# Performance work log

Measured on AMD Instinct MI355X. Metric: run time of the kernel, lower is better.

## Reference

```python
import jax, jax.numpy as jnp
import numpy as np

IN_DIM = 9
HIDDEN = 32
SORT_K = 30


def setup_inputs() -> dict:
    key = jax.random.key(0)
    ks = jax.random.split(key, 16)
    N, E, G = 250000, 2500000, 2048
    x = jax.random.normal(ks[0], (N, IN_DIM), dtype=jnp.float32)
    edge_index = jax.random.randint(ks[1], (2, E), 0, N, dtype=jnp.int32)
    batch = jnp.sort(jax.random.randint(ks[2], (N,), 0, G, dtype=jnp.int32))
    s = lambda k, sh: jax.random.normal(k, sh, dtype=jnp.float32) * 0.05
    return {
        "x": x, "edge_index": edge_index, "batch": batch, "num_graphs": G,
        "W1": s(ks[3], (IN_DIM, HIDDEN)), "b1": jnp.zeros((HIDDEN,), jnp.float32),
        "W2": s(ks[4], (HIDDEN, HIDDEN)), "b2": jnp.zeros((HIDDEN,), jnp.float32),
        "W3": s(ks[5], (HIDDEN, HIDDEN)), "b3": jnp.zeros((HIDDEN,), jnp.float32),
        "cw1": s(ks[6], (16, HIDDEN, 5)), "cb1": jnp.zeros((16,), jnp.float32),
        "cw2": s(ks[7], (32, 16, 5)), "cb2": jnp.zeros((32,), jnp.float32),
        "lw1": s(ks[8], (32 * (SORT_K - 8), 128)), "lb1": jnp.zeros((128,), jnp.float32),
        "lw2": s(ks[9], (128, 1)), "lb2": jnp.zeros((1,), jnp.float32),
    }


def _gcn(x, W, b, src, dst, dis, n):
    # PyG-style GCNConv: sym-normalized A+I, linear transform first.
    h = x @ W                                     # [N, H]
    msg = h[src] * (dis[src] * dis[dst])[:, None]  # [E, H]
    agg = jax.ops.segment_sum(msg, dst, num_segments=n)
    agg = agg + h * (dis * dis)[:, None]           # self-loops
    return agg + b


def _sort_pool(x, batch, num_graphs, k):
    n, h = x.shape
    key = x[:, -1]
    order = jnp.lexsort((-key, batch))             # by graph, key descending
    xs = x[order]
    bs = batch[order]
    counts = jax.ops.segment_sum(jnp.ones((n,), jnp.int32), batch, num_segments=num_graphs)
    starts = jnp.cumsum(counts) - counts           # exclusive prefix sum
    pos = jnp.arange(n, dtype=jnp.int32) - starts[bs]
    valid = pos < k
    g = jnp.where(valid, bs, num_graphs)           # out-of-range -> dropped
    p = jnp.where(valid, pos, 0)
    out = jnp.zeros((num_graphs, k, h), x.dtype)
    return out.at[g, p].set(xs, mode="drop")


def _conv1d(x, w, b):
    # x: [B, C, T], w: [O, I, K]
    y = jax.lax.conv_general_dilated(x, w, window_strides=(1,), padding="VALID",
                                     dimension_numbers=("NCH", "OIH", "NCH"))
    return y + b[None, :, None]


def reference(x, edge_index, batch, num_graphs, W1, b1, W2, b2, W3, b3,
              cw1, cb1, cw2, cb2, lw1, lb1, lw2, lb2):
    n = x.shape[0]
    src, dst = edge_index[0], edge_index[1]
    deg = jax.ops.segment_sum(jnp.ones_like(src, dtype=x.dtype), dst, num_segments=n) + 1.0
    dis = jax.lax.rsqrt(deg)
    h = jax.nn.relu(_gcn(x, W1, b1, src, dst, dis, n))
    h = jax.nn.relu(_gcn(h, W2, b2, src, dst, dis, n))
    h = jax.nn.relu(_gcn(h, W3, b3, src, dst, dis, n))
    p = _sort_pool(h, batch, num_graphs, SORT_K)   # [G, K, H]
    p = jnp.transpose(p, (0, 2, 1))                # [G, H, K]
    p = jax.nn.relu(_conv1d(p, cw1, cb1))
    p = jax.nn.relu(_conv1d(p, cw2, cb2))
    p = p.reshape(num_graphs, -1)
    p = jax.nn.relu(p @ lw1 + lb1)
    return (p @ lw2 + lb2).reshape(-1)
```

## Files before the change

kernel.cpp:

```cpp
#include <hip/hip_runtime.h>

typedef unsigned long long ull;

#define HIDDEN 32
#define SORTK 30
#define KCAP 256
#define GPB 2
#define BSH 7
#define BNODES (1 << BSH)
#define BCAP 1536
#define HMAX 2048
#define NSEG 256
#define SRC_BITS 18
#define SRC_MASK ((1u << SRC_BITS) - 1)
#define EID_SH  SRC_BITS
#define LD_SH   (SRC_BITS + 22)

static inline int ceil_div_i(long long a, int b){ return (int)((a + b - 1) / b); }

__global__ __launch_bounds__(1024) void hist_kernel(const int* __restrict__ dsts,
                                                    int* __restrict__ hist,
                                                    int E, int NB, int segsz){
  __shared__ int h[HMAX];
  for (int i = threadIdx.x; i < NB; i += 1024) h[i] = 0;
  __syncthreads();
  int seg = blockIdx.x;
  int e0 = seg * segsz;
  int e1 = e0 + segsz; if (e1 > E) e1 = E;
  for (int e = e0 + threadIdx.x; e < e1; e += 1024)
    atomicAdd(&h[dsts[e] >> BSH], 1);
  __syncthreads();
  for (int i = threadIdx.x; i < NB; i += 1024) hist[seg * NB + i] = h[i];
}

__global__ __launch_bounds__(256) void segscanA(const int* __restrict__ hist,
                                                int* __restrict__ segoff,
                                                int* __restrict__ btot,
                                                int NB, int S){
  int wv = (blockIdx.x * 256 + threadIdx.x) >> 6;
  int lane = threadIdx.x & 63;
  if (wv >= NB) return;
  int b = wv;
  int run_base = 0;
  for (int chunk = 0; chunk < S; chunk += 64){
    int s = chunk + lane;
    int v = (s < S) ? hist[(size_t)s * NB + b] : 0;
    int x = v;
    #pragma unroll
    for (int o = 1; o < 64; o <<= 1){ int y = __shfl_up(x, o, 64); if (lane >= o) x += y; }
    if (s < S) segoff[(size_t)s * NB + b] = run_base + x - v;
    run_base += __shfl(x, 63, 64);
  }
  if (lane == 0) btot[b] = run_base;
}

__global__ __launch_bounds__(1024) void segscanB(const int* __restrict__ btot,
                                                 int* __restrict__ bbase, int NB){
  int t = threadIdx.x;
  int b0 = t * 2, b1 = t * 2 + 1;
  int v0 = (b0 < NB) ? btot[b0] : 0;
  int v1 = (b1 < NB) ? btot[b1] : 0;
  int pair = v0 + v1;
  int lane = t & 63, wid = t >> 6;
  int x = pair;
  for (int o = 1; o < 64; o <<= 1){ int y = __shfl_up(x, o, 64); if (lane >= o) x += y; }
  __shared__ int wsum[16]; __shared__ int woff[16];
  if (lane == 63) wsum[wid] = x;
  __syncthreads();
  if (t == 0){ int run = 0; for (int w = 0; w < 16; w++){ woff[w] = run; run += wsum[w]; } }
  __syncthreads();
  int excl = x - pair + woff[wid];
  if (b0 < NB) bbase[b0] = excl;
  if (b1 < NB) bbase[b1] = excl + v0;
}

__global__ __launch_bounds__(1024) void scatter_kernel(const int* __restrict__ dsts,
                                                       const int* __restrict__ srcs,
                                                       const int* __restrict__ segoff,
                                                       const int* __restrict__ bbase,
                                                       ull* __restrict__ staging,
                                                       int E, int NB, int segsz){
  __shared__ int cur[HMAX];
  int seg = blockIdx.x;
  for (int i = threadIdx.x; i < NB; i += 1024) cur[i] = segoff[seg * NB + i] + bbase[i];
  __syncthreads();
  int e0 = seg * segsz;
  int e1 = e0 + segsz; if (e1 > E) e1 = E;
  for (int e = e0 + threadIdx.x; e < e1; e += 1024){
    int d = dsts[e];
    int slot = atomicAdd(&cur[d >> BSH], 1);
    staging[slot] = ((ull)(d & (BNODES - 1)) << LD_SH) | ((ull)e << EID_SH)
                  | (ull)(unsigned)srcs[e];
  }
}

__global__ __launch_bounds__(BNODES) void bucket_sort_kernel(
    const int* __restrict__ bbase, const ull* __restrict__ staging,
    int* __restrict__ csr, int* __restrict__ offs,
    float* __restrict__ dis, int N, int NB, int E){
  __shared__ ull ebuf[BCAP];
  __shared__ ull obuf[BCAP];
  __shared__ int cnt[BNODES];
  __shared__ int cur[BNODES];
  __shared__ int w0tot;
  int b = blockIdx.x, t = threadIdx.x;
  int n0 = b << BSH;
  int n1 = n0 + BNODES; if (n1 > N) n1 = N;
  int gbeg = bbase[b];
  int gend = (b + 1 < NB) ? bbase[b + 1] : E;
  int cnt_all = gend - gbeg;
  cnt[t] = 0;
  __syncthreads();

  if (cnt_all <= BCAP){
    for (int i = t; i < cnt_all; i += BNODES){
      ull k = staging[gbeg + i];
      ebuf[i] = k;
      atomicAdd(&cnt[(int)(k >> LD_SH)], 1);
    }
    __syncthreads();
    int v = cnt[t];
    int lane = t & 63, wid = t >> 6;
    int x = v;
    for (int o = 1; o < 64; o <<= 1){ int y = __shfl_up(x, o, 64); if (lane >= o) x += y; }
    if (wid == 0 && lane == 63) w0tot = x;
    __syncthreads();
    int ls = x - v + (wid ? w0tot : 0);
    cur[t] = ls;
    int n = n0 + t;
    if (n < n1){
      float dd = (float)v + 1.0f;
      dis[n]  = __fdiv_rn(1.0f, __fsqrt_rn(dd));
      offs[n] = gbeg + ls;
    }
    __syncthreads();
    for (int i = t; i < cnt_all; i += BNODES){
      ull k = ebuf[i];
      int pos = atomicAdd(&cur[(int)(k >> LD_SH)], 1);
      obuf[pos] = k;
    }
    __syncthreads();
    for (int i = ls + 1; i < ls + v; i++){
      ull k = obuf[i]; int j = i - 1;
      while (j >= ls && obuf[j] > k){ obuf[j + 1] = obuf[j]; j--; }
      obuf[j + 1] = k;
    }
    __syncthreads();
    for (int i = t; i < cnt_all; i += BNODES)
      csr[gbeg + i] = (int)(obuf[i] & SRC_MASK);
  } else {
    int n = n0 + t;
    int deg = 0;
    if (n < n1){
      for (int i = gbeg; i < gend; i++) if ((int)(staging[i] >> LD_SH) == t) deg++;
      float dd = (float)deg + 1.0f;
      dis[n] = __fdiv_rn(1.0f, __fsqrt_rn(dd));
    }
    cnt[t] = (n < n1) ? deg : 0;
    __syncthreads();
    if (n < n1){
      int ls = gbeg; for (int q = 0; q < t; q++) ls += cnt[q];
      offs[n] = ls;
      ull prev = 0;
      for (int o = 0; o < deg; o++){
        ull best = ~0ull;
        for (int i = gbeg; i < gend; i++){
          ull k = staging[i];
          if ((int)(k >> LD_SH) == t && (o == 0 || k > prev) && k < best) best = k;
        }
        csr[ls + o] = (int)(best & SRC_MASK); prev = best;
      }
    }
  }
  if (b == 0 && t == 0) offs[N] = E;
}

template<int K>
__global__ void node_matmul(const float* __restrict__ xin, const float* __restrict__ W,
                            float* __restrict__ H, int N){
  __shared__ float Ws[K * 32];
  for (int i = threadIdx.x; i < K * 32; i += blockDim.x) Ws[i] = W[i];
  __syncthreads();
  int tid = blockIdx.x * blockDim.x + threadIdx.x;
  int n = tid >> 5, c = tid & 31;
  if (n >= N) return;
  const float* xr = xin + (size_t)n * K;
  float acc = 0.f;
  #pragma unroll
  for (int k = 0; k < K; k++) acc = fmaf(xr[k], Ws[k * 32 + c], acc);
  H[(size_t)n * 32 + c] = acc;
}

__device__ __forceinline__ float4 acc_edge(float4 a, float4 h, float w){
  a.x = __fadd_rn(a.x, __fmul_rn(h.x, w));
  a.y = __fadd_rn(a.y, __fmul_rn(h.y, w));
  a.z = __fadd_rn(a.z, __fmul_rn(h.z, w));
  a.w = __fadd_rn(a.w, __fmul_rn(h.w, w));
  return a;
}

__global__ __launch_bounds__(256) void agg_kernel(const float* __restrict__ H,
                           const int* __restrict__ offsets,
                           const int* __restrict__ csr, const float* __restrict__ dis,
                           const float* __restrict__ bias, float* __restrict__ A,
                           float* __restrict__ keyout, int N){
  int tid = blockIdx.x * 256 + threadIdx.x;
  int n = tid >> 3, qw = tid & 7;
  if (n >= N) return;
  const float4* __restrict__ H4 = (const float4*)H;
  float dn = dis[n];
  int s = offsets[n], e = offsets[n + 1];
  float4 acc = make_float4(0.f, 0.f, 0.f, 0.f);
  int i = s;
  for (; i + 4 <= e; i += 4){
    int s0 = csr[i], s1 = csr[i+1], s2 = csr[i+2], s3 = csr[i+3];
    float4 h0 = H4[(size_t)s0 * 8 + qw];
    float4 h1 = H4[(size_t)s1 * 8 + qw];
    float4 h2 = H4[(size_t)s2 * 8 + qw];
    float4 h3 = H4[(size_t)s3 * 8 + qw];
    float w0 = __fmul_rn(dis[s0], dn), w1 = __fmul_rn(dis[s1], dn);
    float w2 = __fmul_rn(dis[s2], dn), w3 = __fmul_rn(dis[s3], dn);
    acc = acc_edge(acc, h0, w0);
    acc = acc_edge(acc, h1, w1);
    acc = acc_edge(acc, h2, w2);
    acc = acc_edge(acc, h3, w3);
  }
  for (; i < e; i++){
    int sr = csr[i];
    float w = __fmul_rn(dis[sr], dn);
    acc = acc_edge(acc, H4[(size_t)sr * 8 + qw], w);
  }
  float4 hn = H4[(size_t)n * 8 + qw];
  float sw = __fmul_rn(dn, dn);
  float4 bb = ((const float4*)bias)[qw];
  float4 v;
  v.x = fmaxf(__fadd_rn(__fadd_rn(acc.x, __fmul_rn(hn.x, sw)), bb.x), 0.f);
  v.y = fmaxf(__fadd_rn(__fadd_rn(acc.y, __fmul_rn(hn.y, sw)), bb.y), 0.f);
  v.z = fmaxf(__fadd_rn(__fadd_rn(acc.z, __fmul_rn(hn.z, sw)), bb.z), 0.f);
  v.w = fmaxf(__fadd_rn(__fadd_rn(acc.w, __fmul_rn(hn.w, sw)), bb.w), 0.f);
  ((float4*)A)[(size_t)n * 8 + qw] = v;
  if (keyout != nullptr && qw == 7) keyout[n] = v.w;
}

__global__ void gstarts_kernel(const int* __restrict__ batch, int* __restrict__ gstarts,
                               int N, int G){
  int g = blockIdx.x * blockDim.x + threadIdx.x;
  if (g > G) return;
  int lo = 0, hi = N;
  while (lo < hi){ int mid = (lo + hi) >> 1; if (batch[mid] < g) lo = mid + 1; else hi = mid; }
  gstarts[g] = lo;
}

__global__ __launch_bounds__(512) void head_kernel(
    const float* __restrict__ A, const float* __restrict__ keys,
    const int* __restrict__ gstarts,
    const float* __restrict__ cw1, const float* __restrict__ cb1,
    const float* __restrict__ cw2, const float* __restrict__ cb2,
    const float* __restrict__ lw1, const float* __restrict__ lb1,
    const float* __restrict__ lw2, const float* __restrict__ lb2,
    float* __restrict__ out, int G){
  int t = threadIdx.x;
  int sub = t >> 8, lt = t & 255;
  int g = blockIdx.x * GPB + sub;

  __shared__ float w1s[16 * 32 * 5];
  __shared__ float w2s[32 * 16 * 5];
  __shared__ float bufA[GPB][960];
  __shared__ float bufB[GPB][416];
  __shared__ int   sel[GPB][SORTK];

  for (int i = t; i < 2560; i += 512) w1s[i] = cw1[i];
  for (int i = t; i < 2560; i += 512) w2s[i] = cw2[i];
  for (int i = lt; i < 960; i += 256) bufA[sub][i] = 0.f;

  bool valid = (g < G);
  int s = 0, c = 0;
  if (valid){ s = gstarts[g]; c = gstarts[g + 1] - s; }
  bool fast = valid && (c <= KCAP);
  if (fast)
    for (int i = lt; i < c; i += 256) bufB[sub][i] = keys[s + i];
  __syncthreads();

  if (valid){
    if (fast){
      for (int i = lt; i < c; i += 256){
        float ki = bufB[sub][i];
        int rank = 0;
        #pragma unroll 8
        for (int j = 0; j < c; j++){
          float kj = bufB[sub][j];
          rank += (kj > ki || (kj == ki && j < i)) ? 1 : 0;
        }
        if (rank < SORTK) sel[sub][rank] = i;
      }
    } else {
      for (int i = lt; i < c; i += 256){
        float ki = keys[s + i];
        int rank = 0;
        for (int j = 0; j < c; j++){
          float kj = keys[s + j];
          if (kj > ki || (kj == ki && j < i)){
            if (++rank >= SORTK) break;
          }
        }
        if (rank < SORTK) sel[sub][rank] = i;
      }
    }
  }
  __syncthreads();

  if (valid){
    int kk = c < SORTK ? c : SORTK;
    for (int q = lt; q < kk * 32; q += 256){
      int pos = q >> 5, ch = q & 31;
      bufA[sub][ch * 30 + pos] = A[(size_t)(s + sel[sub][pos]) * 32 + ch];
    }
  }
  __syncthreads();

  if (valid){
    for (int q = lt; q < 16 * 26; q += 256){
      int o = q / 26, tt = q - o * 26;
      float acc = cb1[o];
      const float* wo = &w1s[o * 160];
      #pragma unroll 4
      for (int i = 0; i < 32; i++){
        const float* si = &bufA[sub][i * 30 + tt];
        #pragma unroll
        for (int k = 0; k < 5; k++) acc = fmaf(si[k], wo[i * 5 + k], acc);
      }
      bufB[sub][q] = fmaxf(acc, 0.f);
    }
  }
  __syncthreads();

  if (valid){
    for (int q = lt; q < 32 * 22; q += 256){
      int o = q / 22, tt = q - o * 22;
      float acc = cb2[o];
      const float* wo = &w2s[o * 80];
      #pragma unroll 4
      for (int i = 0; i < 16; i++){
        const float* si = &bufB[sub][i * 26 + tt];
        #pragma unroll
        for (int k = 0; k < 5; k++) acc = fmaf(si[k], wo[i * 5 + k], acc);
      }
      bufA[sub][q] = fmaxf(acc, 0.f);
    }
  }
  __syncthreads();

  if (valid){
    int outi = lt & 127, half = lt >> 7;
    float acc = half ? 0.f : lb1[outi];
    const int j0 = half * 352;
    #pragma unroll 8
    for (int j = 0; j < 352; j++){
      int jj = j0 + j;
      acc = fmaf(bufA[sub][jj], lw1[(size_t)jj * 128 + outi], acc);
    }
    bufB[sub][half * 128 + outi] = acc;
  }
  __syncthreads();
  if (valid && lt < 128) bufB[sub][lt] = fmaxf(bufB[sub][lt] + bufB[sub][128 + lt], 0.f);
  __syncthreads();

  if (valid && lt < 64){
    float v = __fadd_rn(__fmul_rn(bufB[sub][lt], lw2[lt]),
                        __fmul_rn(bufB[sub][lt + 64], lw2[lt + 64]));
    #pragma unroll
    for (int o = 32; o > 0; o >>= 1) v += __shfl_xor(v, o, 64);
    if (lt == 0) out[g] = v + lb2[0];
  }
}

extern "C" void kernel_launch(void* const* d_in, const int* in_sizes, int n_in,
                              void* d_out, int out_size, void* d_ws, size_t ws_size,
                              hipStream_t stream){
  const float* x     = (const float*)d_in[0];
  const int*   ei    = (const int*)  d_in[1];
  const int*   batch = (const int*)  d_in[2];
  const float* W1  = (const float*)d_in[4];
  const float* b1  = (const float*)d_in[5];
  const float* W2  = (const float*)d_in[6];
  const float* b2  = (const float*)d_in[7];
  const float* W3  = (const float*)d_in[8];
  const float* b3  = (const float*)d_in[9];
  const float* cw1 = (const float*)d_in[10];
  const float* cb1 = (const float*)d_in[11];
  const float* cw2 = (const float*)d_in[12];
  const float* cb2 = (const float*)d_in[13];
  const float* lw1 = (const float*)d_in[14];
  const float* lb1 = (const float*)d_in[15];
  const float* lw2 = (const float*)d_in[16];
  const float* lb2 = (const float*)d_in[17];

  int N = in_sizes[0] / 9;
  int E = in_sizes[1] / 2;
  int G = out_size;
  const int* srcs = ei;
  const int* dsts = ei + E;
  int NB = ceil_div_i(N, BNODES);
  int segsz = ceil_div_i(E, NSEG);

  char* base = (char*)d_ws;
  size_t off = 0;
  auto alloc = [&](size_t bytes) -> void* {
    off = (off + 255) & ~(size_t)255;
    void* r = base + off; off += bytes; return r;
  };
  float* dis    = (float*)alloc((size_t)N * 4);
  float* H      = (float*)alloc((size_t)N * 32 * 4);
  float* A      = (float*)alloc((size_t)N * 32 * 4);
  float* keyarr = (float*)alloc((size_t)N * 4);
  int*   offs   = (int*)alloc((size_t)(N + 1) * 4);
  int*   csr    = (int*)alloc((size_t)E * 4);
  int*   gst    = (int*)alloc((size_t)(G + 1) * 4);
  int*   hist   = (int*)alloc((size_t)NSEG * NB * 4);
  int*   segoff = (int*)alloc((size_t)NSEG * NB * 4);
  int*   btot   = (int*)alloc((size_t)NB * 4);
  int*   bbase  = (int*)alloc((size_t)(NB + 1) * 4);
  ull*   staging = (ull*)H;
  (void)ws_size; (void)n_in;

  hist_kernel<<<NSEG, 1024, 0, stream>>>(dsts, hist, E, NB, segsz);
  segscanA<<<ceil_div_i(NB * 64, 256), 256, 0, stream>>>(hist, segoff, btot, NB, NSEG);
  segscanB<<<1, 1024, 0, stream>>>(btot, bbase, NB);
  scatter_kernel<<<NSEG, 1024, 0, stream>>>(dsts, srcs, segoff, bbase, staging, E, NB, segsz);
  bucket_sort_kernel<<<NB, BNODES, 0, stream>>>(bbase, staging, csr, offs, dis, N, NB, E);

  int ntm = ceil_div_i((long long)N * 32, 256);
  int nta = ceil_div_i((long long)N * 8, 256);
  node_matmul<9><<<ntm, 256, 0, stream>>>(x, W1, H, N);
  agg_kernel<<<nta, 256, 0, stream>>>(H, offs, csr, dis, b1, A, nullptr, N);
  node_matmul<32><<<ntm, 256, 0, stream>>>(A, W2, H, N);
  agg_kernel<<<nta, 256, 0, stream>>>(H, offs, csr, dis, b2, A, nullptr, N);
  node_matmul<32><<<ntm, 256, 0, stream>>>(A, W3, H, N);
  agg_kernel<<<nta, 256, 0, stream>>>(H, offs, csr, dis, b3, A, keyarr, N);

  gstarts_kernel<<<ceil_div_i(G + 1, 256), 256, 0, stream>>>(batch, gst, N, G);
  head_kernel<<<ceil_div_i(G, GPB), 512, 0, stream>>>(A, keyarr, gst, cw1, cb1, cw2, cb2,
                                                      lw1, lb1, lw2, lb2, (float*)d_out, G);
}
```

Baseline: 524.7 us.

## Parallel rank-based bucket sort, float4 node matmul, deeper agg unroll

Replaces the per-thread insertion sort of each node's edge keys with a rank computation where each thread places one edge by counting smaller keys in its node's segment, writing straight to csr. Vectorizes the node matmul input row loads as float4 when K is a multiple of 4. Unrolls the aggregation gather loop to 8 edges to keep more loads in flight. The rank step costs O(deg^2) comparisons per node but spreads them across threads, which removes the serial imbalance of the insertion sort.

New measurement: 551.0 us. +5.0%, slower.

```diff
diff --git a/kernel.cpp b/kernel.cpp
--- a/kernel.cpp
+++ b/kernel.cpp
@@ -102,6 +102,7 @@
   __shared__ ull obuf[BCAP];
   __shared__ int cnt[BNODES];
   __shared__ int cur[BNODES];
+  __shared__ int base0[BNODES];
   __shared__ int w0tot;
   int b = blockIdx.x, t = threadIdx.x;
   int n0 = b << BSH;
@@ -127,6 +128,7 @@
     __syncthreads();
     int ls = x - v + (wid ? w0tot : 0);
     cur[t] = ls;
+    base0[t] = ls;
     int n = n0 + t;
     if (n < n1){
       float dd = (float)v + 1.0f;
@@ -140,14 +142,15 @@
       obuf[pos] = k;
     }
     __syncthreads();
-    for (int i = ls + 1; i < ls + v; i++){
-      ull k = obuf[i]; int j = i - 1;
-      while (j >= ls && obuf[j] > k){ obuf[j + 1] = obuf[j]; j--; }
-      obuf[j + 1] = k;
-    }
-    __syncthreads();
-    for (int i = t; i < cnt_all; i += BNODES)
-      csr[gbeg + i] = (int)(obuf[i] & SRC_MASK);
+    for (int i = t; i < cnt_all; i += BNODES){
+      ull k = obuf[i];
+      int nd = (int)(k >> LD_SH);
+      int base = base0[nd];
+      int vn = cnt[nd];
+      int r = 0;
+      for (int j = 0; j < vn; j++) r += (obuf[base + j] < k) ? 1 : 0;
+      csr[gbeg + base + r] = (int)(k & SRC_MASK);
+    }
   } else {
     int n = n0 + t;
     int deg = 0;
@@ -186,8 +189,20 @@
   if (n >= N) return;
   const float* xr = xin + (size_t)n * K;
   float acc = 0.f;
-  #pragma unroll
-  for (int k = 0; k < K; k++) acc = fmaf(xr[k], Ws[k * 32 + c], acc);
+  if constexpr ((K & 3) == 0){
+    const float4* xr4 = (const float4*)xr;
+    #pragma unroll
+    for (int k4 = 0; k4 < K / 4; k4++){
+      float4 xv = xr4[k4];
+      acc = fmaf(xv.x, Ws[(k4 * 4 + 0) * 32 + c], acc);
+      acc = fmaf(xv.y, Ws[(k4 * 4 + 1) * 32 + c], acc);
+      acc = fmaf(xv.z, Ws[(k4 * 4 + 2) * 32 + c], acc);
+      acc = fmaf(xv.w, Ws[(k4 * 4 + 3) * 32 + c], acc);
+    }
+  } else {
+    #pragma unroll
+    for (int k = 0; k < K; k++) acc = fmaf(xr[k], Ws[k * 32 + c], acc);
+  }
   H[(size_t)n * 32 + c] = acc;
 }
 
@@ -212,18 +227,29 @@
   int s = offsets[n], e = offsets[n + 1];
   float4 acc = make_float4(0.f, 0.f, 0.f, 0.f);
   int i = s;
-  for (; i + 4 <= e; i += 4){
-    int s0 = csr[i], s1 = csr[i+1], s2 = csr[i+2], s3 = csr[i+3];
+  for (; i + 8 <= e; i += 8){
+    int s0 = csr[i],   s1 = csr[i+1], s2 = csr[i+2], s3 = csr[i+3];
+    int s4 = csr[i+4], s5 = csr[i+5], s6 = csr[i+6], s7 = csr[i+7];
     float4 h0 = H4[(size_t)s0 * 8 + qw];
     float4 h1 = H4[(size_t)s1 * 8 + qw];
     float4 h2 = H4[(size_t)s2 * 8 + qw];
     float4 h3 = H4[(size_t)s3 * 8 + qw];
+    float4 h4 = H4[(size_t)s4 * 8 + qw];
+    float4 h5 = H4[(size_t)s5 * 8 + qw];
+    float4 h6 = H4[(size_t)s6 * 8 + qw];
+    float4 h7 = H4[(size_t)s7 * 8 + qw];
     float w0 = __fmul_rn(dis[s0], dn), w1 = __fmul_rn(dis[s1], dn);
     float w2 = __fmul_rn(dis[s2], dn), w3 = __fmul_rn(dis[s3], dn);
+    float w4 = __fmul_rn(dis[s4], dn), w5 = __fmul_rn(dis[s5], dn);
+    float w6 = __fmul_rn(dis[s6], dn), w7 = __fmul_rn(dis[s7], dn);
     acc = acc_edge(acc, h0, w0);
     acc = acc_edge(acc, h1, w1);
     acc = acc_edge(acc, h2, w2);
     acc = acc_edge(acc, h3, w3);
+    acc = acc_edge(acc, h4, w4);
+    acc = acc_edge(acc, h5, w5);
+    acc = acc_edge(acc, h6, w6);
+    acc = acc_edge(acc, h7, w7);
   }
   for (; i < e; i++){
     int sr = csr[i];
```
